# Optimization experiments

Measured on AMD Instinct MI355X. Metric: run time of the kernel, lower is better.

The kernel has to match this reference:

```python
import jax, jax.numpy as jnp
import numpy as np

N_RAW, N1, N2, K, D, OUT = 200000, 100000, 20000, 10, 256, 256

def setup_inputs() -> dict:
    key = jax.random.key(0)
    ks = jax.random.split(key, 8)
    scale1 = (6.0 / (OUT + 2 * D)) ** 0.5   # xavier_uniform bound
    scale2 = (6.0 / (OUT + 2 * OUT)) ** 0.5
    return {
        "raw_features": jax.random.normal(ks[0], (N_RAW, D), dtype=jnp.float32),
        "W1": jax.random.uniform(ks[1], (OUT, 2 * D), jnp.float32, -scale1, scale1),
        "W2": jax.random.uniform(ks[2], (OUT, 2 * OUT), jnp.float32, -scale2, scale2),
        "nodes1": jax.random.randint(ks[3], (N1,), 0, N_RAW),
        "neigh1": jax.random.randint(ks[4], (N1, K), 0, N_RAW),
        "self2": jax.random.randint(ks[5], (N2,), 0, N1),
        "neigh2": jax.random.randint(ks[6], (N2, K), 0, N1),
    }

def _sage_layer(embs, self_idx, neigh_idx, W):
    # segment-mean over sampled neighbors (MEAN agg with fixed fanout K)
    agg = jnp.mean(embs[neigh_idx], axis=1)          # [n, d]
    combined = jnp.concatenate([embs[self_idx], agg], axis=1)  # [n, 2d]
    # F.relu(W.mm(combined.t())).t() == relu(combined @ W.T)
    return jax.nn.relu(combined @ W.T)

def reference(raw_features, W1, W2, nodes1, neigh1, self2, neigh2):
    h1 = _sage_layer(raw_features, nodes1, neigh1, W1)  # [N1, OUT]
    h2 = _sage_layer(h1, self2, neigh2, W2)             # [N2, OUT]
    return h2
```

## Files before the change

kernel.cpp:

```cpp
#include <hip/hip_runtime.h>
#include <hip/hip_bf16.h>


typedef __attribute__((ext_vector_type(8))) short bf16x8;
typedef __attribute__((ext_vector_type(4))) float f32x4;

__device__ __forceinline__ short f2bf(float f) {
  __hip_bfloat16 h = __float2bfloat16(f);
  return *reinterpret_cast<short*>(&h);
}
__device__ __forceinline__ float bf2f(short s) {
  union { unsigned u; float f; } x;
  x.u = ((unsigned)(unsigned short)s) << 16;
  return x.f;
}

__global__ __launch_bounds__(256) void convert_w(const float* __restrict__ w,
                                                 short* __restrict__ wb, int n) {
  int i = blockIdx.x * 256 + threadIdx.x;
  if (i < n) wb[i] = f2bf(w[i]);
}

__global__ __launch_bounds__(256) void convert_raw(const float* __restrict__ in,
                                                   short* __restrict__ out) {
  const size_t i = (size_t)blockIdx.x * 256 + threadIdx.x;
  const float4* in4 = reinterpret_cast<const float4*>(in);
  float4 u = in4[i * 2], v = in4[i * 2 + 1];
  bf16x8 o;
  o[0] = f2bf(u.x); o[1] = f2bf(u.y); o[2] = f2bf(u.z); o[3] = f2bf(u.w);
  o[4] = f2bf(v.x); o[5] = f2bf(v.y); o[6] = f2bf(v.z); o[7] = f2bf(v.w);
  reinterpret_cast<bf16x8*>(out)[i] = o;
}

template <bool OUT_BF16>
__global__ __launch_bounds__(256) void sage_fused(
    const short* __restrict__ E,
    const int* __restrict__ self_idx,
    const int* __restrict__ neigh,
    const short* __restrict__ Wb,
    void* __restrict__ out,
    int Nvalid) {
  __shared__ short As[32][520];

  const int tid = threadIdx.x;
  const int m0 = blockIdx.x * 32;

  {
    const int c = tid & 31;
    const int rs = tid >> 5;
#pragma unroll
    for (int rr = 0; rr < 4; ++rr) {
      const int r = rs * 4 + rr;
      const int gr = m0 + r;
      if (gr < Nvalid) {
        const int si = self_idx[gr];
        bf16x8 sv = *reinterpret_cast<const bf16x8*>(E + (size_t)si * 256 + c * 8);
        float a0 = 0.f, a1 = 0.f, a2 = 0.f, a3 = 0.f,
              a4 = 0.f, a5 = 0.f, a6 = 0.f, a7 = 0.f;
#pragma unroll
        for (int k = 0; k < 10; ++k) {
          const int nb = neigh[(size_t)gr * 10 + k];
          bf16x8 v = *reinterpret_cast<const bf16x8*>(E + (size_t)nb * 256 + c * 8);
          a0 += bf2f(v[0]); a1 += bf2f(v[1]); a2 += bf2f(v[2]); a3 += bf2f(v[3]);
          a4 += bf2f(v[4]); a5 += bf2f(v[5]); a6 += bf2f(v[6]); a7 += bf2f(v[7]);
        }
        bf16x8 mv;
        mv[0] = f2bf(a0 * 0.1f); mv[1] = f2bf(a1 * 0.1f);
        mv[2] = f2bf(a2 * 0.1f); mv[3] = f2bf(a3 * 0.1f);
        mv[4] = f2bf(a4 * 0.1f); mv[5] = f2bf(a5 * 0.1f);
        mv[6] = f2bf(a6 * 0.1f); mv[7] = f2bf(a7 * 0.1f);
        *reinterpret_cast<bf16x8*>(&As[r][c * 8]) = sv;
        *reinterpret_cast<bf16x8*>(&As[r][256 + c * 8]) = mv;
      } else {
        bf16x8 z = {0, 0, 0, 0, 0, 0, 0, 0};
        *reinterpret_cast<bf16x8*>(&As[r][c * 8]) = z;
        *reinterpret_cast<bf16x8*>(&As[r][256 + c * 8]) = z;
      }
    }
  }
  __syncthreads();

  const int wave = tid >> 6, lane = tid & 63;
  const int wn = wave * 64;
  const int lr = lane & 15;
  const int lkb = (lane >> 4) * 8;

  f32x4 acc[2][4] = {};

#pragma unroll 2
  for (int k0 = 0; k0 < 512; k0 += 32) {
    bf16x8 a0 = *reinterpret_cast<const bf16x8*>(&As[lr][k0 + lkb]);
    bf16x8 a1 = *reinterpret_cast<const bf16x8*>(&As[16 + lr][k0 + lkb]);
    bf16x8 b0 = *reinterpret_cast<const bf16x8*>(Wb + (size_t)(wn + 0 + lr) * 512 + k0 + lkb);
    bf16x8 b1 = *reinterpret_cast<const bf16x8*>(Wb + (size_t)(wn + 16 + lr) * 512 + k0 + lkb);
    bf16x8 b2 = *reinterpret_cast<const bf16x8*>(Wb + (size_t)(wn + 32 + lr) * 512 + k0 + lkb);
    bf16x8 b3 = *reinterpret_cast<const bf16x8*>(Wb + (size_t)(wn + 48 + lr) * 512 + k0 + lkb);

    acc[0][0] = __builtin_amdgcn_mfma_f32_16x16x32_bf16(a0, b0, acc[0][0], 0, 0, 0);
    acc[1][0] = __builtin_amdgcn_mfma_f32_16x16x32_bf16(a1, b0, acc[1][0], 0, 0, 0);
    acc[0][1] = __builtin_amdgcn_mfma_f32_16x16x32_bf16(a0, b1, acc[0][1], 0, 0, 0);
    acc[1][1] = __builtin_amdgcn_mfma_f32_16x16x32_bf16(a1, b1, acc[1][1], 0, 0, 0);
    acc[0][2] = __builtin_amdgcn_mfma_f32_16x16x32_bf16(a0, b2, acc[0][2], 0, 0, 0);
    acc[1][2] = __builtin_amdgcn_mfma_f32_16x16x32_bf16(a1, b2, acc[1][2], 0, 0, 0);
    acc[0][3] = __builtin_amdgcn_mfma_f32_16x16x32_bf16(a0, b3, acc[0][3], 0, 0, 0);
    acc[1][3] = __builtin_amdgcn_mfma_f32_16x16x32_bf16(a1, b3, acc[1][3], 0, 0, 0);
  }

#pragma unroll
  for (int mi = 0; mi < 2; ++mi)
#pragma unroll
    for (int ni = 0; ni < 4; ++ni)
#pragma unroll
      for (int r = 0; r < 4; ++r) {
        const int gm = m0 + mi * 16 + (lane >> 4) * 4 + r;
        const int gn = wn + ni * 16 + lr;
        float v = acc[mi][ni][r];
        v = v > 0.f ? v : 0.f;
        if (gm < Nvalid) {
          if (OUT_BF16)
            reinterpret_cast<short*>(out)[(size_t)gm * 256 + gn] = f2bf(v);
          else
            reinterpret_cast<float*>(out)[(size_t)gm * 256 + gn] = v;
        }
      }
}

extern "C" void kernel_launch(void* const* d_in, const int* in_sizes, int n_in,
                              void* d_out, int out_size, void* d_ws, size_t ws_size,
                              hipStream_t stream) {
  const float* raw = (const float*)d_in[0];
  const float* W1 = (const float*)d_in[1];
  const float* W2 = (const float*)d_in[2];
  const int* nodes1 = (const int*)d_in[3];
  const int* neigh1 = (const int*)d_in[4];
  const int* self2 = (const int*)d_in[5];
  const int* neigh2 = (const int*)d_in[6];
  float* out = (float*)d_out;

  const int N_RAW = 200000, N1 = 100000, N2 = 20000;

  short* rawb = (short*)d_ws;
  short* h1 = rawb + (size_t)N_RAW * 256;
  short* W1b = h1 + (size_t)N1 * 256;
  short* W2b = W1b + 131072;

  convert_w<<<512, 256, 0, stream>>>(W1, W1b, 131072);
  convert_w<<<512, 256, 0, stream>>>(W2, W2b, 131072);
  convert_raw<<<(N_RAW * 256 / 8) / 256, 256, 0, stream>>>(raw, rawb);

  sage_fused<true><<<N1 / 32, 256, 0, stream>>>(rawb, nodes1, neigh1, W1b, h1, N1);
  sage_fused<false><<<N2 / 32, 256, 0, stream>>>(h1, self2, neigh2, W2b, out, N2);
}
```

Before: 244.4 us.

## Merge conversion kernels, batch gather loads, and software-pipeline MFMA operand loads

Result: faster. 226.0 us (-7.5%).

```diff
diff --git a/kernel.cpp b/kernel.cpp
--- a/kernel.cpp
+++ b/kernel.cpp
@@ -5,41 +5,43 @@
 typedef __attribute__((ext_vector_type(8))) short bf16x8;
 typedef __attribute__((ext_vector_type(4))) float f32x4;
 
-__device__ __forceinline__ short f2bf(float f) {
+static __device__ __forceinline__ short f2bf(float f) {
   __hip_bfloat16 h = __float2bfloat16(f);
   return *reinterpret_cast<short*>(&h);
 }
-__device__ __forceinline__ float bf2f(short s) {
+static __device__ __forceinline__ float bf2f(short s) {
   union { unsigned u; float f; } x;
   x.u = ((unsigned)(unsigned short)s) << 16;
   return x.f;
 }
 
-__global__ __launch_bounds__(256) void convert_w(const float* __restrict__ w,
-                                                 short* __restrict__ wb, int n) {
-  int i = blockIdx.x * 256 + threadIdx.x;
-  if (i < n) wb[i] = f2bf(w[i]);
-}
-
-__global__ __launch_bounds__(256) void convert_raw(const float* __restrict__ in,
-                                                   short* __restrict__ out) {
-  const size_t i = (size_t)blockIdx.x * 256 + threadIdx.x;
-  const float4* in4 = reinterpret_cast<const float4*>(in);
-  float4 u = in4[i * 2], v = in4[i * 2 + 1];
+__global__ __launch_bounds__(256) void convert_all(
+    const float* __restrict__ raw, const float* __restrict__ W1,
+    const float* __restrict__ W2, short* __restrict__ rawb,
+    short* __restrict__ W1b, short* __restrict__ W2b) {
+  const int b = blockIdx.x;
+  const float* src;
+  short* dst;
+  size_t base;
+  if (b < 25000) { src = raw; dst = rawb; base = (size_t)b * 2048; }
+  else if (b < 25064) { src = W1; dst = W1b; base = (size_t)(b - 25000) * 2048; }
+  else { src = W2; dst = W2b; base = (size_t)(b - 25064) * 2048; }
+  const size_t i = base + (size_t)threadIdx.x * 8;
+  const float4* s4 = reinterpret_cast<const float4*>(src + i);
+  float4 u = s4[0], v = s4[1];
   bf16x8 o;
   o[0] = f2bf(u.x); o[1] = f2bf(u.y); o[2] = f2bf(u.z); o[3] = f2bf(u.w);
   o[4] = f2bf(v.x); o[5] = f2bf(v.y); o[6] = f2bf(v.z); o[7] = f2bf(v.w);
-  reinterpret_cast<bf16x8*>(out)[i] = o;
+  *reinterpret_cast<bf16x8*>(dst + i) = o;
 }
 
 template <bool OUT_BF16>
-__global__ __launch_bounds__(256) void sage_fused(
+__global__ __launch_bounds__(256, 4) void sage_fused(
     const short* __restrict__ E,
     const int* __restrict__ self_idx,
     const int* __restrict__ neigh,
     const short* __restrict__ Wb,
-    void* __restrict__ out,
-    int Nvalid) {
+    void* __restrict__ out) {
   __shared__ short As[32][520];
 
   const int tid = threadIdx.x;
@@ -52,30 +54,24 @@
     for (int rr = 0; rr < 4; ++rr) {
       const int r = rs * 4 + rr;
       const int gr = m0 + r;
-      if (gr < Nvalid) {
-        const int si = self_idx[gr];
-        bf16x8 sv = *reinterpret_cast<const bf16x8*>(E + (size_t)si * 256 + c * 8);
-        float a0 = 0.f, a1 = 0.f, a2 = 0.f, a3 = 0.f,
-              a4 = 0.f, a5 = 0.f, a6 = 0.f, a7 = 0.f;
+      const int si = self_idx[gr];
+      int nb[10];
 #pragma unroll
-        for (int k = 0; k < 10; ++k) {
-          const int nb = neigh[(size_t)gr * 10 + k];
-          bf16x8 v = *reinterpret_cast<const bf16x8*>(E + (size_t)nb * 256 + c * 8);
-          a0 += bf2f(v[0]); a1 += bf2f(v[1]); a2 += bf2f(v[2]); a3 += bf2f(v[3]);
-          a4 += bf2f(v[4]); a5 += bf2f(v[5]); a6 += bf2f(v[6]); a7 += bf2f(v[7]);
-        }
-        bf16x8 mv;
-        mv[0] = f2bf(a0 * 0.1f); mv[1] = f2bf(a1 * 0.1f);
-        mv[2] = f2bf(a2 * 0.1f); mv[3] = f2bf(a3 * 0.1f);
-        mv[4] = f2bf(a4 * 0.1f); mv[5] = f2bf(a5 * 0.1f);
-        mv[6] = f2bf(a6 * 0.1f); mv[7] = f2bf(a7 * 0.1f);
-        *reinterpret_cast<bf16x8*>(&As[r][c * 8]) = sv;
-        *reinterpret_cast<bf16x8*>(&As[r][256 + c * 8]) = mv;
-      } else {
-        bf16x8 z = {0, 0, 0, 0, 0, 0, 0, 0};
-        *reinterpret_cast<bf16x8*>(&As[r][c * 8]) = z;
-        *reinterpret_cast<bf16x8*>(&As[r][256 + c * 8]) = z;
+      for (int k = 0; k < 10; ++k) nb[k] = neigh[gr * 10 + k];
+      bf16x8 sv = *reinterpret_cast<const bf16x8*>(E + (size_t)si * 256 + c * 8);
+      bf16x8 v[10];
+#pragma unroll
+      for (int k = 0; k < 10; ++k)
+        v[k] = *reinterpret_cast<const bf16x8*>(E + (size_t)nb[k] * 256 + c * 8);
+      bf16x8 mv;
+#pragma unroll
+      for (int j = 0; j < 8; ++j) {
+        float sA = bf2f(v[0][j]) + bf2f(v[2][j]) + bf2f(v[4][j]) + bf2f(v[6][j]) + bf2f(v[8][j]);
+        float sB = bf2f(v[1][j]) + bf2f(v[3][j]) + bf2f(v[5][j]) + bf2f(v[7][j]) + bf2f(v[9][j]);
+        mv[j] = f2bf((sA + sB) * 0.1f);
       }
+      *reinterpret_cast<bf16x8*>(&As[r][c * 8]) = sv;
+      *reinterpret_cast<bf16x8*>(&As[r][256 + c * 8]) = mv;
     }
   }
   __syncthreads();
@@ -84,18 +80,30 @@
   const int wn = wave * 64;
   const int lr = lane & 15;
   const int lkb = (lane >> 4) * 8;
+  const short* Bp = Wb + (size_t)(wn + lr) * 512 + lkb;
 
   f32x4 acc[2][4] = {};
 
-#pragma unroll 2
-  for (int k0 = 0; k0 < 512; k0 += 32) {
-    bf16x8 a0 = *reinterpret_cast<const bf16x8*>(&As[lr][k0 + lkb]);
-    bf16x8 a1 = *reinterpret_cast<const bf16x8*>(&As[16 + lr][k0 + lkb]);
-    bf16x8 b0 = *reinterpret_cast<const bf16x8*>(Wb + (size_t)(wn + 0 + lr) * 512 + k0 + lkb);
-    bf16x8 b1 = *reinterpret_cast<const bf16x8*>(Wb + (size_t)(wn + 16 + lr) * 512 + k0 + lkb);
-    bf16x8 b2 = *reinterpret_cast<const bf16x8*>(Wb + (size_t)(wn + 32 + lr) * 512 + k0 + lkb);
-    bf16x8 b3 = *reinterpret_cast<const bf16x8*>(Wb + (size_t)(wn + 48 + lr) * 512 + k0 + lkb);
+  bf16x8 a0 = *reinterpret_cast<const bf16x8*>(&As[lr][lkb]);
+  bf16x8 a1 = *reinterpret_cast<const bf16x8*>(&As[16 + lr][lkb]);
+  bf16x8 b0 = *reinterpret_cast<const bf16x8*>(Bp + 0 * 8192);
+  bf16x8 b1 = *reinterpret_cast<const bf16x8*>(Bp + 1 * 8192);
+  bf16x8 b2 = *reinterpret_cast<const bf16x8*>(Bp + 2 * 8192);
+  bf16x8 b3 = *reinterpret_cast<const bf16x8*>(Bp + 3 * 8192);
 
+#pragma unroll
+  for (int ks = 0; ks < 16; ++ks) {
+    bf16x8 na0, na1, nb0, nb1, nb2, nb3;
+    if (ks < 15) {
+      const int k0 = (ks + 1) * 32;
+      na0 = *reinterpret_cast<const bf16x8*>(&As[lr][k0 + lkb]);
+      na1 = *reinterpret_cast<const bf16x8*>(&As[16 + lr][k0 + lkb]);
+      nb0 = *reinterpret_cast<const bf16x8*>(Bp + k0 + 0 * 8192);
+      nb1 = *reinterpret_cast<const bf16x8*>(Bp + k0 + 1 * 8192);
+      nb2 = *reinterpret_cast<const bf16x8*>(Bp + k0 + 2 * 8192);
+      nb3 = *reinterpret_cast<const bf16x8*>(Bp + k0 + 3 * 8192);
+    }
+    __builtin_amdgcn_s_setprio(1);
     acc[0][0] = __builtin_amdgcn_mfma_f32_16x16x32_bf16(a0, b0, acc[0][0], 0, 0, 0);
     acc[1][0] = __builtin_amdgcn_mfma_f32_16x16x32_bf16(a1, b0, acc[1][0], 0, 0, 0);
     acc[0][1] = __builtin_amdgcn_mfma_f32_16x16x32_bf16(a0, b1, acc[0][1], 0, 0, 0);
@@ -104,6 +112,8 @@
     acc[1][2] = __builtin_amdgcn_mfma_f32_16x16x32_bf16(a1, b2, acc[1][2], 0, 0, 0);
     acc[0][3] = __builtin_amdgcn_mfma_f32_16x16x32_bf16(a0, b3, acc[0][3], 0, 0, 0);
     acc[1][3] = __builtin_amdgcn_mfma_f32_16x16x32_bf16(a1, b3, acc[1][3], 0, 0, 0);
+    __builtin_amdgcn_s_setprio(0);
+    a0 = na0; a1 = na1; b0 = nb0; b1 = nb1; b2 = nb2; b3 = nb3;
   }
 
 #pragma unroll
@@ -116,12 +126,10 @@
         const int gn = wn + ni * 16 + lr;
         float v = acc[mi][ni][r];
         v = v > 0.f ? v : 0.f;
-        if (gm < Nvalid) {
-          if (OUT_BF16)
-            reinterpret_cast<short*>(out)[(size_t)gm * 256 + gn] = f2bf(v);
-          else
-            reinterpret_cast<float*>(out)[(size_t)gm * 256 + gn] = v;
-        }
+        if (OUT_BF16)
+          reinterpret_cast<short*>(out)[(size_t)gm * 256 + gn] = f2bf(v);
+        else
+          reinterpret_cast<float*>(out)[(size_t)gm * 256 + gn] = v;
       }
 }
 
@@ -144,10 +152,7 @@
   short* W1b = h1 + (size_t)N1 * 256;
   short* W2b = W1b + 131072;
 
-  convert_w<<<512, 256, 0, stream>>>(W1, W1b, 131072);
-  convert_w<<<512, 256, 0, stream>>>(W2, W2b, 131072);
-  convert_raw<<<(N_RAW * 256 / 8) / 256, 256, 0, stream>>>(raw, rawb);
-
-  sage_fused<true><<<N1 / 32, 256, 0, stream>>>(rawb, nodes1, neigh1, W1b, h1, N1);
-  sage_fused<false><<<N2 / 32, 256, 0, stream>>>(h1, self2, neigh2, W2b, out, N2);
+  convert_all<<<25128, 256, 0, stream>>>(raw, W1, W2, rawb, W1b, W2b);
+  sage_fused<true><<<N1 / 32, 256, 0, stream>>>(rawb, nodes1, neigh1, W1b, h1);
+  sage_fused<false><<<N2 / 32, 256, 0, stream>>>(h1, self2, neigh2, W2b, out);
 }
```
